# Kernel optimization log

Hardware: AMD Instinct MI355X
Metric: run time of the kernel (lower is better)

## Reference

```python
import jax, jax.numpy as jnp
import numpy as np

E, D_IN, D_OUT, A, R, T = 8, 1024, 1024, 4, 16, 8192


def setup_inputs() -> dict:
    key = jax.random.key(0)
    ks = jax.random.split(key, 6)
    x = jax.random.normal(ks[0], (T, D_IN), jnp.float32)
    weight = jax.random.normal(ks[1], (E, D_IN, D_OUT), jnp.float32) / np.float32(np.sqrt(D_IN))
    # he_uniform-like scale for lora_A; lora_B random (zeros in real init would hide the LoRA path)
    lora_A = jax.random.normal(ks[2], (A, E, D_IN, R), jnp.float32) * np.float32(np.sqrt(2.0 / D_IN))
    lora_B = jax.random.normal(ks[3], (A, E, R, D_OUT), jnp.float32) * np.float32(0.02)
    lora_scaling = jax.random.uniform(ks[4], (A,), jnp.float32, 0.5, 1.5)
    group_sizes = jnp.full((E,), T // E, dtype=jnp.int32)  # sums to T
    adapter_indices_sorted = jax.random.randint(ks[5], (T,), 0, A, dtype=jnp.int32)
    return {
        'x': x, 'weight': weight, 'lora_A': lora_A, 'lora_B': lora_B,
        'lora_scaling': lora_scaling, 'group_sizes': group_sizes,
        'adapter_indices_sorted': adapter_indices_sorted,
    }


def reference(x, weight, lora_A, lora_B, lora_scaling, group_sizes, adapter_indices_sorted):
    total_tokens, d_in = x.shape
    n_experts, _, d_out = weight.shape
    n_adapters, _, _, rank = lora_A.shape
    n_groups = n_adapters * n_experts

    # Base expert-grouped GEMM: x is already sorted by expert via group_sizes.
    base_out = jax.lax.ragged_dot(x, weight, group_sizes)  # [T, d_out]

    # Combined (adapter, expert) group id per token.
    expert_idx = jnp.repeat(jnp.arange(n_experts), group_sizes, total_repeat_length=total_tokens)
    flat_idx = adapter_indices_sorted * n_experts + expert_idx  # [T]

    # prepare_routing: stable sort tokens by combined group id.
    sort_idx = jnp.argsort(flat_idx, stable=True)
    x_sorted = x[sort_idx]
    combined_group_sizes = jnp.zeros((n_groups,), jnp.int32).at[flat_idx].add(1)
    unsort_idx = jnp.argsort(sort_idx)

    # Nested LoRA grouped GEMMs over flattened (adapter, expert) groups.
    lora_A_flat = lora_A.reshape(n_groups, d_in, rank)
    lora_B_flat = lora_B.reshape(n_groups, rank, d_out)
    intermediate = jax.lax.ragged_dot(x_sorted, lora_A_flat, combined_group_sizes)  # [T, rank]
    lora_out_sorted = jax.lax.ragged_dot(intermediate, lora_B_flat, combined_group_sizes)  # [T, d_out]

    lora_out = lora_out_sorted[unsort_idx] * lora_scaling[adapter_indices_sorted, None]
    return base_out + lora_out
```

## Files before the change

### kernel.cpp

```cpp
#include <hip/hip_runtime.h>
#include <hip/hip_bf16.h>
#include <stdint.h>


#define T_TOK 8192
#define DIN   1024
#define DOUT  1024
#define NE    8
#define NA    4
#define RK    16
#define KEXT  1088
#define NOCT  136

typedef __attribute__((ext_vector_type(8))) short short8;
typedef __attribute__((ext_vector_type(4))) float f32x4;

__device__ __forceinline__ ushort f2bf(float f) {
  union { float f; uint32_t i; } v; v.f = f;
  uint32_t x = v.i;
  return (ushort)((x + 0x7fffu + ((x >> 16) & 1u)) >> 16);
}

__device__ __forceinline__ void gload_lds16(const void* g, void* l) {
  __builtin_amdgcn_global_load_lds(
      (const __attribute__((address_space(1))) uint32_t*)g,
      (__attribute__((address_space(3))) uint32_t*)l,
      16, 0, 0);
}

__device__ __forceinline__ int expert_of_row(const int* __restrict__ gs, int row) {
  int cum = 0, e = 0;
#pragma unroll
  for (int i = 0; i < NE; ++i) { if (row >= cum) e = i; cum += gs[i]; }
  return e;
}

__global__ __launch_bounds__(256) void k_prep(
    const float* __restrict__ weight,
    const float* __restrict__ lora_A, const float* __restrict__ lora_B,
    const float* __restrict__ lora_scaling,
    ushort* __restrict__ Aoct, ushort* __restrict__ Boct) {
  const int bid = blockIdx.x;
  const int tid = threadIdx.x;

  if (bid < 256) {
    int u = bid * 4 + (tid >> 6);
    int e = u >> 7, ko = u & 127;
    int c = tid & 63;
    int a = c >> 4, r = c & 15;
    float s = lora_scaling[a];
    ushort o8[8];
#pragma unroll
    for (int j = 0; j < 8; ++j) {
      float v = lora_A[((size_t)(a * NE + e) * DIN + ko * 8 + j) * RK + r];
      o8[j] = f2bf(s * v);
    }
    *(uint4*)(Aoct + ((size_t)((e * 128 + ko) * 64 + c)) * 8) = *(const uint4*)o8;
  } else {
    int e, ko;
    const float* srcbase;
    int stride;
    if (bid < 1280) {
      int u = bid - 256;
      e = u >> 7; ko = u & 127;
      srcbase = weight + (size_t)e * DIN * DOUT + (size_t)(ko * 8) * DOUT;
      stride = DOUT;
    } else {
      int u = bid - 1280;
      e = u >> 3; int o = u & 7; ko = 128 + o;
      srcbase = nullptr; stride = 0;
    }
    int n4 = tid * 4;
    float v[8][4];
    if (bid < 1280) {
#pragma unroll
      for (int j = 0; j < 8; ++j) {
        float4 q = *(const float4*)(srcbase + (size_t)j * stride + n4);
        v[j][0] = q.x; v[j][1] = q.y; v[j][2] = q.z; v[j][3] = q.w;
      }
    } else {
      int o = ko - 128;
#pragma unroll
      for (int j = 0; j < 8; ++j) {
        int kv = o * 8 + j;
        int a = kv >> 4, r = kv & 15;
        float4 q = *(const float4*)(lora_B + (size_t)((a * NE + e) * RK + r) * DOUT + n4);
        v[j][0] = q.x; v[j][1] = q.y; v[j][2] = q.z; v[j][3] = q.w;
      }
    }
    ushort* dst = Boct + ((size_t)(e * NOCT + ko) * DOUT + n4) * 8;
#pragma unroll
    for (int i = 0; i < 4; ++i) {
      ushort o8[8];
#pragma unroll
      for (int j = 0; j < 8; ++j) o8[j] = f2bf(v[j][i]);
      *(uint4*)(dst + i * 8) = *(const uint4*)o8;
    }
  }
}

__global__ __launch_bounds__(256) void k_xva(
    const float* __restrict__ x, ushort* __restrict__ xp,
    const ushort* __restrict__ Aoct,
    const int* __restrict__ gs, const int* __restrict__ adapter_idx) {
  __shared__ ushort As2[64 * 64];
  __shared__ ushort Bs2[8 * 64 * 8];

  const int tid = threadIdx.x;
  const int lane = tid & 63;
  const int wave = tid >> 6;
  const int rows0 = blockIdx.x * 64;
  const int e = expert_of_row(gs, rows0);
  const ushort* aoct = Aoct + (size_t)e * 128 * 64 * 8;

  const int row = tid >> 2;
  const int seg = tid & 3;
  const int r7 = row & 7;
  const int c0 = seg * 2;

  f32x4 acc[4];
#pragma unroll
  for (int ni = 0; ni < 4; ++ni) acc[ni] = (f32x4){0.f, 0.f, 0.f, 0.f};

  for (int kt = 0; kt < 16; ++kt) {
#pragma unroll
    for (int rd = 0; rd < 2; ++rd) {
      int o = wave * 2 + rd;
      const ushort* src = aoct + ((size_t)(kt * 8 + o) * 64 + lane) * 8;
      gload_lds16(src, &Bs2[o * 64 * 8]);
    }

    const float* srcx = x + (size_t)(rows0 + row) * DIN + kt * 64 + seg * 16;
    float4 q0 = ((const float4*)srcx)[0];
    float4 q1 = ((const float4*)srcx)[1];
    float4 q2 = ((const float4*)srcx)[2];
    float4 q3 = ((const float4*)srcx)[3];
    ushort o16[16];
    o16[0] = f2bf(q0.x); o16[1] = f2bf(q0.y); o16[2] = f2bf(q0.z); o16[3] = f2bf(q0.w);
    o16[4] = f2bf(q1.x); o16[5] = f2bf(q1.y); o16[6] = f2bf(q1.z); o16[7] = f2bf(q1.w);
    o16[8]  = f2bf(q2.x); o16[9]  = f2bf(q2.y); o16[10] = f2bf(q2.z); o16[11] = f2bf(q2.w);
    o16[12] = f2bf(q3.x); o16[13] = f2bf(q3.y); o16[14] = f2bf(q3.z); o16[15] = f2bf(q3.w);

    ushort* dstg = xp + (size_t)(rows0 + row) * KEXT + kt * 64 + seg * 16;
    *(uint4*)(dstg)     = ((const uint4*)o16)[0];
    *(uint4*)(dstg + 8) = ((const uint4*)o16)[1];

    *(uint4*)&As2[row * 64 + ((c0 ^ r7) * 8)]       = ((const uint4*)o16)[0];
    *(uint4*)&As2[row * 64 + (((c0 + 1) ^ r7) * 8)] = ((const uint4*)o16)[1];

    __syncthreads();

    int m = wave * 16 + (lane & 15);
#pragma unroll
    for (int h = 0; h < 2; ++h) {
      int kblk = h * 4 + (lane >> 4);
      short8 af = *(const short8*)&As2[m * 64 + (kblk ^ (m & 7)) * 8];
#pragma unroll
      for (int ni = 0; ni < 4; ++ni) {
        short8 bfv = *(const short8*)&Bs2[(kblk * 64 + ni * 16 + (lane & 15)) * 8];
        acc[ni] = __builtin_amdgcn_mfma_f32_16x16x32_bf16(af, bfv, acc[ni], 0, 0, 0);
      }
    }
    __syncthreads();
  }

#pragma unroll
  for (int i = 0; i < 4; ++i) {
    int grow = rows0 + wave * 16 + (lane >> 4) * 4 + i;
    int a_row = adapter_idx[grow];
#pragma unroll
    for (int ni = 0; ni < 4; ++ni) {
      float val = (a_row == ni) ? acc[ni][i] : 0.f;
      xp[(size_t)grow * KEXT + DIN + ni * 16 + (lane & 15)] = f2bf(val);
    }
  }
}

__global__ __launch_bounds__(256) void k_gemm(
    const ushort* __restrict__ xp, const ushort* __restrict__ Boct,
    const int* __restrict__ gs, float* __restrict__ out) {
  __shared__ ushort As[128 * 64];
  __shared__ ushort Bs[8 * 128 * 8];

  const int tid = threadIdx.x;
  const int lane = tid & 63;
  const int wave = tid >> 6;
  const int wm = wave >> 1, wn = wave & 1;

  const int bid = blockIdx.x;
  const int swz = (bid & 7) * 64 + (bid >> 3);
  const int row0 = (swz >> 3) * 128;
  const int n0 = (swz & 7) * 128;
  const int e = expert_of_row(gs, row0);
  const ushort* boct = Boct + (size_t)e * NOCT * DOUT * 8;

  f32x4 acc[4][4];
#pragma unroll
  for (int mi = 0; mi < 4; ++mi)
#pragma unroll
    for (int ni = 0; ni < 4; ++ni) acc[mi][ni] = (f32x4){0.f, 0.f, 0.f, 0.f};

  const int r8 = lane >> 3;
  const int c8s = (lane & 7) ^ r8;

  for (int kt = 0; kt < 17; ++kt) {
#pragma unroll
    for (int rd = 0; rd < 4; ++rd) {
      int r = wave * 32 + rd * 8 + r8;
      const ushort* src = xp + (size_t)(row0 + r) * KEXT + kt * 64 + c8s * 8;
      gload_lds16(src, &As[(wave * 32 + rd * 8) * 64]);
    }
#pragma unroll
    for (int rd = 0; rd < 4; ++rd) {
      int u = wave * 4 + rd;
      int o = u >> 1, hf = u & 1;
      const ushort* src = boct + ((size_t)(kt * 8 + o) * DOUT + n0 + hf * 64 + lane) * 8;
      gload_lds16(src, &Bs[(o * 128 + hf * 64) * 8]);
    }
    __syncthreads();

#pragma unroll
    for (int h = 0; h < 2; ++h) {
      int kblk = h * 4 + (lane >> 4);
      short8 af[4], bfv[4];
#pragma unroll
      for (int mi = 0; mi < 4; ++mi) {
        int m = wm * 64 + mi * 16 + (lane & 15);
        af[mi] = *(const short8*)&As[m * 64 + (kblk ^ (m & 7)) * 8];
      }
#pragma unroll
      for (int ni = 0; ni < 4; ++ni) {
        int n = wn * 64 + ni * 16 + (lane & 15);
        bfv[ni] = *(const short8*)&Bs[(kblk * 128 + n) * 8];
      }
#pragma unroll
      for (int mi = 0; mi < 4; ++mi)
#pragma unroll
        for (int ni = 0; ni < 4; ++ni)
          acc[mi][ni] = __builtin_amdgcn_mfma_f32_16x16x32_bf16(
              af[mi], bfv[ni], acc[mi][ni], 0, 0, 0);
    }
    __syncthreads();
  }

#pragma unroll
  for (int mi = 0; mi < 4; ++mi) {
#pragma unroll
    for (int ni = 0; ni < 4; ++ni) {
      int col = n0 + wn * 64 + ni * 16 + (lane & 15);
#pragma unroll
      for (int i = 0; i < 4; ++i) {
        int r = row0 + wm * 64 + mi * 16 + (lane >> 4) * 4 + i;
        out[(size_t)r * DOUT + col] = acc[mi][ni][i];
      }
    }
  }
}

extern "C" void kernel_launch(void* const* d_in, const int* in_sizes, int n_in,
                              void* d_out, int out_size, void* d_ws, size_t ws_size,
                              hipStream_t stream) {
  const float* x            = (const float*)d_in[0];
  const float* weight       = (const float*)d_in[1];
  const float* lora_A       = (const float*)d_in[2];
  const float* lora_B       = (const float*)d_in[3];
  const float* lora_scaling = (const float*)d_in[4];
  const int*   group_sizes  = (const int*)d_in[5];
  const int*   adapter_idx  = (const int*)d_in[6];
  float* out = (float*)d_out;

  const size_t sz_xp    = (size_t)T_TOK * KEXT * 2;
  const size_t sz_boct  = (size_t)NE * NOCT * DOUT * 8 * 2;
  ushort* xp   = (ushort*)d_ws;
  ushort* boct = (ushort*)((char*)d_ws + sz_xp);
  ushort* aoct = (ushort*)((char*)d_ws + sz_xp + sz_boct);

  k_prep<<<1344, 256, 0, stream>>>(weight, lora_A, lora_B, lora_scaling,
                                   aoct, boct);
  k_xva<<<T_TOK / 64, 256, 0, stream>>>(x, xp, aoct, group_sizes, adapter_idx);
  k_gemm<<<512, 256, 0, stream>>>(xp, boct, group_sizes, out);
}
```

Measured before the change: 162.5 us.

## Split A-prep into own kernel and co-schedule x·A with weight conversion

The prep kernel is split so that only the small lora_A conversion runs first. The x-to-bf16 conversion plus the x·A LoRA projection is then merged into the same launch as the weight and lora_B conversion, so the two independent memory-bound tasks run concurrently. The x·A part now uses 16-row blocks (512 blocks) instead of 64-row blocks, giving more parallelism. The cost is more redundant Aoct loads per row and smaller MFMA work per block.

```diff
diff --git a/kernel.cpp b/kernel.cpp
--- a/kernel.cpp
+++ b/kernel.cpp
@@ -35,47 +35,103 @@
   return e;
 }
 
-__global__ __launch_bounds__(256) void k_prep(
-    const float* __restrict__ weight,
-    const float* __restrict__ lora_A, const float* __restrict__ lora_B,
-    const float* __restrict__ lora_scaling,
-    ushort* __restrict__ Aoct, ushort* __restrict__ Boct) {
+__global__ __launch_bounds__(256) void k_prepA(
+    const float* __restrict__ lora_A, const float* __restrict__ lora_scaling,
+    ushort* __restrict__ Aoct) {
   const int bid = blockIdx.x;
   const int tid = threadIdx.x;
-
-  if (bid < 256) {
-    int u = bid * 4 + (tid >> 6);
-    int e = u >> 7, ko = u & 127;
-    int c = tid & 63;
-    int a = c >> 4, r = c & 15;
-    float s = lora_scaling[a];
-    ushort o8[8];
-#pragma unroll
-    for (int j = 0; j < 8; ++j) {
-      float v = lora_A[((size_t)(a * NE + e) * DIN + ko * 8 + j) * RK + r];
-      o8[j] = f2bf(s * v);
-    }
-    *(uint4*)(Aoct + ((size_t)((e * 128 + ko) * 64 + c)) * 8) = *(const uint4*)o8;
+  int u = bid * 4 + (tid >> 6);
+  int e = u >> 7, ko = u & 127;
+  int c = tid & 63;
+  int a = c >> 4, r = c & 15;
+  float s = lora_scaling[a];
+  ushort o8[8];
+#pragma unroll
+  for (int j = 0; j < 8; ++j) {
+    float v = lora_A[((size_t)(a * NE + e) * DIN + ko * 8 + j) * RK + r];
+    o8[j] = f2bf(s * v);
+  }
+  *(uint4*)(Aoct + ((size_t)((e * 128 + ko) * 64 + c)) * 8) = *(const uint4*)o8;
+}
+
+__global__ __launch_bounds__(256) void k_main(
+    const float* __restrict__ x, ushort* __restrict__ xp,
+    const ushort* __restrict__ Aoct,
+    const float* __restrict__ weight, const float* __restrict__ lora_B,
+    ushort* __restrict__ Boct,
+    const int* __restrict__ gs, const int* __restrict__ adapter_idx) {
+  __shared__ ushort As2[16 * 64];
+  __shared__ ushort Bs2[8 * 64 * 8];
+
+  const int bid = blockIdx.x;
+  const int tid = threadIdx.x;
+
+  if (bid < 512) {
+    const int lane = tid & 63;
+    const int wave = tid >> 6;
+    const int rows0 = bid * 16;
+    const int e = expert_of_row(gs, rows0);
+    const ushort* aoct = Aoct + (size_t)e * 128 * 64 * 8;
+
+    const int row = tid >> 4;
+    const int seg = tid & 15;
+    const int r7 = row & 7;
+
+    f32x4 acc = (f32x4){0.f, 0.f, 0.f, 0.f};
+
+    for (int kt = 0; kt < 16; ++kt) {
+#pragma unroll
+      for (int rd = 0; rd < 2; ++rd) {
+        int o = wave * 2 + rd;
+        const ushort* src = aoct + ((size_t)(kt * 8 + o) * 64 + lane) * 8;
+        gload_lds16(src, &Bs2[o * 64 * 8]);
+      }
+
+      const float* srcx = x + (size_t)(rows0 + row) * DIN + kt * 64 + seg * 4;
+      float4 q = *(const float4*)srcx;
+      ushort4 b;
+      b.x = f2bf(q.x); b.y = f2bf(q.y); b.z = f2bf(q.z); b.w = f2bf(q.w);
+      *(ushort4*)(xp + (size_t)(rows0 + row) * KEXT + kt * 64 + seg * 4) = b;
+      int ch = (seg >> 1) ^ r7;
+      *(ushort4*)&As2[row * 64 + ch * 8 + (seg & 1) * 4] = b;
+
+      __syncthreads();
+
+      int m = lane & 15;
+#pragma unroll
+      for (int h = 0; h < 2; ++h) {
+        int kblk = h * 4 + (lane >> 4);
+        short8 af = *(const short8*)&As2[m * 64 + (kblk ^ (m & 7)) * 8];
+        short8 bfv = *(const short8*)&Bs2[(kblk * 64 + wave * 16 + m) * 8];
+        acc = __builtin_amdgcn_mfma_f32_16x16x32_bf16(af, bfv, acc, 0, 0, 0);
+      }
+      __syncthreads();
+    }
+
+#pragma unroll
+    for (int i = 0; i < 4; ++i) {
+      int grow = rows0 + (lane >> 4) * 4 + i;
+      int a_row = adapter_idx[grow];
+      float val = (a_row == wave) ? acc[i] : 0.f;
+      xp[(size_t)grow * KEXT + DIN + wave * 16 + (lane & 15)] = f2bf(val);
+    }
   } else {
     int e, ko;
-    const float* srcbase;
-    int stride;
-    if (bid < 1280) {
-      int u = bid - 256;
+    const float* srcbase = nullptr;
+    if (bid < 1536) {
+      int u = bid - 512;
       e = u >> 7; ko = u & 127;
       srcbase = weight + (size_t)e * DIN * DOUT + (size_t)(ko * 8) * DOUT;
-      stride = DOUT;
     } else {
-      int u = bid - 1280;
+      int u = bid - 1536;
       e = u >> 3; int o = u & 7; ko = 128 + o;
-      srcbase = nullptr; stride = 0;
     }
     int n4 = tid * 4;
     float v[8][4];
-    if (bid < 1280) {
+    if (bid < 1536) {
 #pragma unroll
       for (int j = 0; j < 8; ++j) {
-        float4 q = *(const float4*)(srcbase + (size_t)j * stride + n4);
+        float4 q = *(const float4*)(srcbase + (size_t)j * DOUT + n4);
         v[j][0] = q.x; v[j][1] = q.y; v[j][2] = q.z; v[j][3] = q.w;
       }
     } else {
@@ -95,83 +151,6 @@
 #pragma unroll
       for (int j = 0; j < 8; ++j) o8[j] = f2bf(v[j][i]);
       *(uint4*)(dst + i * 8) = *(const uint4*)o8;
-    }
-  }
-}
-
-__global__ __launch_bounds__(256) void k_xva(
-    const float* __restrict__ x, ushort* __restrict__ xp,
-    const ushort* __restrict__ Aoct,
-    const int* __restrict__ gs, const int* __restrict__ adapter_idx) {
-  __shared__ ushort As2[64 * 64];
-  __shared__ ushort Bs2[8 * 64 * 8];
-
-  const int tid = threadIdx.x;
-  const int lane = tid & 63;
-  const int wave = tid >> 6;
-  const int rows0 = blockIdx.x * 64;
-  const int e = expert_of_row(gs, rows0);
-  const ushort* aoct = Aoct + (size_t)e * 128 * 64 * 8;
-
-  const int row = tid >> 2;
-  const int seg = tid & 3;
-  const int r7 = row & 7;
-  const int c0 = seg * 2;
-
-  f32x4 acc[4];
-#pragma unroll
-  for (int ni = 0; ni < 4; ++ni) acc[ni] = (f32x4){0.f, 0.f, 0.f, 0.f};
-
-  for (int kt = 0; kt < 16; ++kt) {
-#pragma unroll
-    for (int rd = 0; rd < 2; ++rd) {
-      int o = wave * 2 + rd;
-      const ushort* src = aoct + ((size_t)(kt * 8 + o) * 64 + lane) * 8;
-      gload_lds16(src, &Bs2[o * 64 * 8]);
-    }
-
-    const float* srcx = x + (size_t)(rows0 + row) * DIN + kt * 64 + seg * 16;
-    float4 q0 = ((const float4*)srcx)[0];
-    float4 q1 = ((const float4*)srcx)[1];
-    float4 q2 = ((const float4*)srcx)[2];
-    float4 q3 = ((const float4*)srcx)[3];
-    ushort o16[16];
-    o16[0] = f2bf(q0.x); o16[1] = f2bf(q0.y); o16[2] = f2bf(q0.z); o16[3] = f2bf(q0.w);
-    o16[4] = f2bf(q1.x); o16[5] = f2bf(q1.y); o16[6] = f2bf(q1.z); o16[7] = f2bf(q1.w);
-    o16[8]  = f2bf(q2.x); o16[9]  = f2bf(q2.y); o16[10] = f2bf(q2.z); o16[11] = f2bf(q2.w);
-    o16[12] = f2bf(q3.x); o16[13] = f2bf(q3.y); o16[14] = f2bf(q3.z); o16[15] = f2bf(q3.w);
-
-    ushort* dstg = xp + (size_t)(rows0 + row) * KEXT + kt * 64 + seg * 16;
-    *(uint4*)(dstg)     = ((const uint4*)o16)[0];
-    *(uint4*)(dstg + 8) = ((const uint4*)o16)[1];
-
-    *(uint4*)&As2[row * 64 + ((c0 ^ r7) * 8)]       = ((const uint4*)o16)[0];
-    *(uint4*)&As2[row * 64 + (((c0 + 1) ^ r7) * 8)] = ((const uint4*)o16)[1];
-
-    __syncthreads();
-
-    int m = wave * 16 + (lane & 15);
-#pragma unroll
-    for (int h = 0; h < 2; ++h) {
-      int kblk = h * 4 + (lane >> 4);
-      short8 af = *(const short8*)&As2[m * 64 + (kblk ^ (m & 7)) * 8];
-#pragma unroll
-      for (int ni = 0; ni < 4; ++ni) {
-        short8 bfv = *(const short8*)&Bs2[(kblk * 64 + ni * 16 + (lane & 15)) * 8];
-        acc[ni] = __builtin_amdgcn_mfma_f32_16x16x32_bf16(af, bfv, acc[ni], 0, 0, 0);
-      }
-    }
-    __syncthreads();
-  }
-
-#pragma unroll
-  for (int i = 0; i < 4; ++i) {
-    int grow = rows0 + wave * 16 + (lane >> 4) * 4 + i;
-    int a_row = adapter_idx[grow];
-#pragma unroll
-    for (int ni = 0; ni < 4; ++ni) {
-      float val = (a_row == ni) ? acc[ni][i] : 0.f;
-      xp[(size_t)grow * KEXT + DIN + ni * 16 + (lane & 15)] = f2bf(val);
     }
   }
 }
@@ -275,8 +254,8 @@
   ushort* boct = (ushort*)((char*)d_ws + sz_xp);
   ushort* aoct = (ushort*)((char*)d_ws + sz_xp + sz_boct);
 
-  k_prep<<<1344, 256, 0, stream>>>(weight, lora_A, lora_B, lora_scaling,
-                                   aoct, boct);
-  k_xva<<<T_TOK / 64, 256, 0, stream>>>(x, xp, aoct, group_sizes, adapter_idx);
+  k_prepA<<<256, 256, 0, stream>>>(lora_A, lora_scaling, aoct);
+  k_main<<<1600, 256, 0, stream>>>(x, xp, aoct, weight, lora_B, boct,
+                                   group_sizes, adapter_idx);
   k_gemm<<<512, 256, 0, stream>>>(xp, boct, group_sizes, out);
 }
```

Measured after the change: 159.2 us. 2.0% less time.
